# Performance work log

Measured on AMD Instinct MI355X. Metric: run time of the kernel, lower is better.

## Reference

```python
import jax, jax.numpy as jnp
import numpy as np

QMIN, QMAX = -128.0, 127.0  # int8 fake-quant range for activations
BIAS_ZP = 128.0             # zero point for the uint8-stored quantized bias


def ste_fake_quant(x, scale, zp):
    # scaled fake-quantize: q = clip(round(x/s) + zp, qmin, qmax); deq = (q - zp) * s
    q = jnp.clip(jnp.round(x / scale) + zp, QMIN, QMAX)
    deq = (q - zp) * scale
    # straight-through estimator (matches torch fake_quantize semantics)
    return x + jax.lax.stop_gradient(deq - x)


def setup_inputs() -> dict:
    key = jax.random.key(0)
    ks = jax.random.split(key, 8)
    B, S, K, N, G = 8, 8192, 1024, 1024, 128
    NG = K // G  # groups per output channel
    x = jax.random.normal(ks[0], (B, S, K), dtype=jnp.float32)
    w_q = jax.random.randint(ks[1], (N, K), 0, 16, dtype=jnp.int32)          # int4 codes
    w_scale = jax.random.uniform(ks[2], (N, NG), dtype=jnp.float32) * 0.02 + 1e-3
    w_zp = jax.random.randint(ks[3], (N, NG), 0, 16, dtype=jnp.int32)
    bias_q = jax.random.randint(ks[4], (N,), 0, 256, dtype=jnp.int32)        # uint8 codes
    bias_scale = jax.random.uniform(ks[5], (N,), dtype=jnp.float32) * 0.01 + 1e-4
    in_scale = jax.random.uniform(ks[6], (1,), dtype=jnp.float32) * 0.02 + 0.01
    in_zp = jnp.zeros((1,), dtype=jnp.int32)
    out_scale = jax.random.uniform(ks[7], (1,), dtype=jnp.float32) * 0.2 + 0.05
    out_zp = jnp.zeros((1,), dtype=jnp.int32)
    return {"x": x, "w_q": w_q, "w_scale": w_scale, "w_zp": w_zp,
            "bias_q": bias_q, "bias_scale": bias_scale,
            "in_scale": in_scale, "in_zp": in_zp,
            "out_scale": out_scale, "out_zp": out_zp}


def reference(x, w_q, w_scale, w_zp, bias_q, bias_scale, in_scale, in_zp, out_scale, out_zp):
    dt = x.dtype
    N, K = w_q.shape
    NG = w_scale.shape[1]
    G = K // NG
    # group-wise weight dequantize: [N, K] -> [N, NG, G]
    wq = w_q.reshape(N, NG, G).astype(dt)
    W = ((wq - w_zp[:, :, None].astype(dt)) * w_scale[:, :, None].astype(dt)).reshape(N, K)
    # per-channel bias dequantize
    bias = (bias_q.astype(dt) - BIAS_ZP) * bias_scale.astype(dt)
    # per-tensor fake-quantize of the input activation
    xq = ste_fake_quant(x, in_scale.astype(dt), in_zp.astype(dt))
    # func_method: linear
    out = jnp.einsum('bsk,nk->bsn', xq, W) + bias
    # per-tensor fake-quantize of the output
    return ste_fake_quant(out, out_scale.astype(dt), out_zp.astype(dt))
```

## Files before the change

kernel.cpp:

```cpp
#include <hip/hip_runtime.h>
#include <hip/hip_bf16.h>
#include <stdint.h>

#define M_DIM 65536
#define K_DIM 1024
#define N_DIM 1024
#define NGRP  8

#define T_BM 128
#define T_BN 128
#define T_BK 64
#define T_NKT (K_DIM / T_BK)

#define FB_BM 128
#define FB_BN 128
#define FB_BK 32
#define FB_NKT (K_DIM / FB_BK)

typedef float f32x4 __attribute__((ext_vector_type(4)));
typedef int   ix4   __attribute__((ext_vector_type(4)));
typedef __bf16 bf16x8 __attribute__((ext_vector_type(8)));

__global__ void prep_wd_kernel(const int* __restrict__ w_q,
                               const int* __restrict__ w_zp,
                               const int* __restrict__ bias_q,
                               const float* __restrict__ bias_scale,
                               int8_t* __restrict__ Wd,
                               float* __restrict__ bias_f) {
    const int n = blockIdx.x;
    const int t = threadIdx.x;
    const int k0 = t * 4;
    const int g = k0 >> 7;
    const int zp = w_zp[n * NGRP + g];
    const int4 wq = *reinterpret_cast<const int4*>(w_q + (size_t)n * K_DIM + k0);
    union { int u; int8_t b[4]; } pk;
    pk.b[0] = (int8_t)(wq.x - zp);
    pk.b[1] = (int8_t)(wq.y - zp);
    pk.b[2] = (int8_t)(wq.z - zp);
    pk.b[3] = (int8_t)(wq.w - zp);
    *reinterpret_cast<int*>(Wd + (size_t)n * K_DIM + k0) = pk.u;
    if (t == 0) bias_f[n] = ((float)bias_q[n] - 128.0f) * bias_scale[n];
}

__global__ __launch_bounds__(256) void prep_x8_kernel(
    const float* __restrict__ x,
    const float* __restrict__ in_scale_p, const int* __restrict__ in_zp_p,
    int8_t* __restrict__ Xq)
{
    const float s = in_scale_p[0];
    const float inv = 1.0f / s;
    const float zp = (float)in_zp_p[0];
    const size_t i = ((size_t)blockIdx.x * 256 + threadIdx.x) * 16;
    float vv[16];
#pragma unroll
    for (int c = 0; c < 4; ++c) {
        const float4 v = *reinterpret_cast<const float4*>(x + i + c * 4);
        vv[c * 4 + 0] = v.x; vv[c * 4 + 1] = v.y;
        vv[c * 4 + 2] = v.z; vv[c * 4 + 3] = v.w;
    }
    union { int4 u; int8_t b[16]; } pk;
#pragma unroll
    for (int e = 0; e < 16; ++e) {
        float q = rintf(vv[e] * inv) + zp;
        q = fminf(fmaxf(q, -128.0f), 127.0f);
        pk.b[e] = (int8_t)(q - zp);
    }
    *reinterpret_cast<int4*>(Xq + i) = pk.u;
}

__global__ __launch_bounds__(256, 3) void gemm128_i8_kernel(
    const int8_t* __restrict__ Xq,
    const int8_t* __restrict__ Wd,
    const float* __restrict__ w_scale,
    const float* __restrict__ bias_f,
    const float* __restrict__ in_scale_p,
    const float* __restrict__ out_scale_p, const int* __restrict__ out_zp_p,
    float* __restrict__ out)
{
    __shared__ __align__(16) int8_t Abuf[2][T_BM * T_BK];
    __shared__ __align__(16) int8_t Bbuf[2][T_BN * T_BK];
    __shared__ float WS[NGRP * T_BN];

    const int t = threadIdx.x;
    const int bid = (blockIdx.x & 7) * 512 + (blockIdx.x >> 3);
    const int nt = bid & 7;
    const int mt = bid >> 3;
    const int m0 = mt * T_BM;
    const int n0 = nt * T_BN;

    const int wid = t >> 6;
    const int lane = t & 63;
    const int wr = wid >> 1, wc = wid & 1;
    const int lrow = lane & 15;
    const int kslot = lane >> 4;
    const int koff = ((kslot ^ ((lrow >> 1) & 3)) << 4);
    const int widoff = wid * 1024;

    const int8_t* Abase = Xq + (size_t)m0 * K_DIM;
    const int8_t* Bbase = Wd + (size_t)n0 * K_DIM;

    {
        const int nl = t >> 1;
        const int g4 = (t & 1) * 4;
        const float4 wv = *reinterpret_cast<const float4*>(
            w_scale + (size_t)(n0 + nl) * NGRP + g4);
        WS[(g4 + 0) * T_BN + nl] = wv.x;
        WS[(g4 + 1) * T_BN + nl] = wv.y;
        WS[(g4 + 2) * T_BN + nl] = wv.z;
        WS[(g4 + 3) * T_BN + nl] = wv.w;
    }

    auto stage = [&](int8_t* dst, const int8_t* panel, int kt) {
        const int k0 = kt * T_BK;
#pragma unroll
        for (int j = 0; j < 2; ++j) {
            const int c = j * 256 + t;
            const int r = c >> 2;
            const int sl = (c & 3) ^ ((r >> 1) & 3);
            const int8_t* src = panel + (size_t)r * K_DIM + k0 + sl * 16;
            __builtin_amdgcn_global_load_lds(
                (const __attribute__((address_space(1))) void*)src,
                (__attribute__((address_space(3))) void*)(dst + j * 4096 + widoff),
                16, 0, 0);
        }
    };

    f32x4 facc[4][4];
#pragma unroll
    for (int mi = 0; mi < 4; ++mi)
#pragma unroll
        for (int ni = 0; ni < 4; ++ni)
            facc[mi][ni] = (f32x4){0.f, 0.f, 0.f, 0.f};

    stage(&Abuf[0][0], Abase, 0);
    stage(&Bbuf[0][0], Bbase, 0);
    __syncthreads();

    int buf = 0;
#pragma unroll 1
    for (int kt = 0; kt < T_NKT; ++kt) {
        if (kt + 1 < T_NKT) {
            stage(&Abuf[buf ^ 1][0], Abase, kt + 1);
            stage(&Bbuf[buf ^ 1][0], Bbase, kt + 1);
        }

        ix4 af[4], bfr[4];
#pragma unroll
        for (int i = 0; i < 4; ++i) {
            const int arow = wr * 64 + i * 16 + lrow;
            af[i] = *reinterpret_cast<const ix4*>(&Abuf[buf][arow * 64 + koff]);
        }
#pragma unroll
        for (int i = 0; i < 4; ++i) {
            const int brow = wc * 64 + i * 16 + lrow;
            bfr[i] = *reinterpret_cast<const ix4*>(&Bbuf[buf][brow * 64 + koff]);
        }

        const int g = kt >> 1;
        float wsv[4];
#pragma unroll
        for (int ni = 0; ni < 4; ++ni)
            wsv[ni] = WS[g * T_BN + wc * 64 + ni * 16 + lrow];

#pragma unroll
        for (int mi = 0; mi < 4; ++mi) {
            ix4 s0 = __builtin_amdgcn_mfma_i32_16x16x64_i8(af[mi], bfr[0], (ix4){0,0,0,0}, 0, 0, 0);
            ix4 s1 = __builtin_amdgcn_mfma_i32_16x16x64_i8(af[mi], bfr[1], (ix4){0,0,0,0}, 0, 0, 0);
            ix4 s2 = __builtin_amdgcn_mfma_i32_16x16x64_i8(af[mi], bfr[2], (ix4){0,0,0,0}, 0, 0, 0);
            ix4 s3 = __builtin_amdgcn_mfma_i32_16x16x64_i8(af[mi], bfr[3], (ix4){0,0,0,0}, 0, 0, 0);
#pragma unroll
            for (int e = 0; e < 4; ++e) {
                facc[mi][0][e] += wsv[0] * (float)s0[e];
                facc[mi][1][e] += wsv[1] * (float)s1[e];
                facc[mi][2][e] += wsv[2] * (float)s2[e];
                facc[mi][3][e] += wsv[3] * (float)s3[e];
            }
        }

        __syncthreads();
        buf ^= 1;
    }

    const float in_s  = in_scale_p[0];
    const float out_s = out_scale_p[0];
    const float out_inv = 1.0f / out_s;
    const float ozp = (float)out_zp_p[0];
    const int col = lane & 15;
    const int rgrp = lane >> 4;
#pragma unroll
    for (int ni = 0; ni < 4; ++ni) {
        const int n = n0 + wc * 64 + ni * 16 + col;
        const float bv = bias_f[n];
#pragma unroll
        for (int mi = 0; mi < 4; ++mi) {
#pragma unroll
            for (int j = 0; j < 4; ++j) {
                const int m = m0 + wr * 64 + mi * 16 + rgrp * 4 + j;
                float v = in_s * facc[mi][ni][j] + bv;
                float q = rintf(v * out_inv) + ozp;
                q = fminf(fmaxf(q, -128.0f), 127.0f);
                out[(size_t)m * N_DIM + n] = (q - ozp) * out_s;
            }
        }
    }
}

__global__ void prep_kernel(const int* __restrict__ w_q,
                            const float* __restrict__ w_scale,
                            const int* __restrict__ w_zp,
                            const int* __restrict__ bias_q,
                            const float* __restrict__ bias_scale,
                            __hip_bfloat16* __restrict__ Wb,
                            float* __restrict__ bias_f) {
    const int n = blockIdx.x;
    const int t = threadIdx.x;
    const int k0 = t * 4;
    const int g = k0 >> 7;
    const float s  = w_scale[n * NGRP + g];
    const float zp = (float)w_zp[n * NGRP + g];
    const int4 wq = *reinterpret_cast<const int4*>(w_q + (size_t)n * K_DIM + k0);
    union { ushort4 u; __hip_bfloat16 h[4]; } pk;
    pk.h[0] = __float2bfloat16(((float)wq.x - zp) * s);
    pk.h[1] = __float2bfloat16(((float)wq.y - zp) * s);
    pk.h[2] = __float2bfloat16(((float)wq.z - zp) * s);
    pk.h[3] = __float2bfloat16(((float)wq.w - zp) * s);
    *reinterpret_cast<ushort4*>(Wb + (size_t)n * K_DIM + k0) = pk.u;
    if (t == 0) bias_f[n] = ((float)bias_q[n] - 128.0f) * bias_scale[n];
}

__global__ __launch_bounds__(256) void gemm_fused_kernel(
    const float* __restrict__ x,
    const __hip_bfloat16* __restrict__ Wb,
    const float* __restrict__ bias_f,
    const float* __restrict__ in_scale_p, const int* __restrict__ in_zp_p,
    const float* __restrict__ out_scale_p, const int* __restrict__ out_zp_p,
    float* __restrict__ out)
{
    __shared__ __align__(16) __hip_bfloat16 As[2][FB_BM][FB_BK];
    __shared__ __align__(16) __hip_bfloat16 Bs[2][FB_BN][FB_BK];

    const int t = threadIdx.x;
    const int bid = blockIdx.x;
    const int nt = bid & 7;
    const int mt = bid >> 3;
    const int m0 = mt * FB_BM;
    const int n0 = nt * FB_BN;

    const int wid = t >> 6;
    const int lane = t & 63;
    const int wr = wid >> 1, wc = wid & 1;
    const int lrow = lane & 15;
    const int kslot = lane >> 4;

    const float in_s = in_scale_p[0];
    const float in_inv = 1.0f / in_s;
    const float izp = (float)in_zp_p[0];

    auto stageB = [&](int b, int kt) {
        const int k0 = kt * FB_BK;
#pragma unroll
        for (int j = 0; j < 2; ++j) {
            const int c = (wid * 2 + j) * 64 + lane;
            const int row = c >> 2;
            const int slot = c & 3;
            const __hip_bfloat16* src = Wb + (size_t)(n0 + row) * K_DIM + k0 + slot * 8;
            __builtin_amdgcn_global_load_lds(
                (const __attribute__((address_space(1))) void*)src,
                (__attribute__((address_space(3))) void*)((char*)&Bs[b][0][0] + (wid * 2 + j) * 1024),
                16, 0, 0);
        }
    };
    auto stageA = [&](int b, int kt) {
        const int k0 = kt * FB_BK;
#pragma unroll
        for (int i = 0; i < 4; ++i) {
            const int c = t + 256 * i;
            const int row = c >> 3;
            const int slot = c & 7;
            const float4 v = *reinterpret_cast<const float4*>(
                x + (size_t)(m0 + row) * K_DIM + k0 + slot * 4);
            float vv[4] = {v.x, v.y, v.z, v.w};
            union { ushort4 u; __hip_bfloat16 h[4]; } pk;
#pragma unroll
            for (int e = 0; e < 4; ++e) {
                float q = rintf(vv[e] * in_inv) + izp;
                q = fminf(fmaxf(q, -128.0f), 127.0f);
                pk.h[e] = __float2bfloat16((q - izp) * in_s);
            }
            *reinterpret_cast<ushort4*>(&As[b][row][slot * 4]) = pk.u;
        }
    };

    f32x4 acc[4][4];
#pragma unroll
    for (int mi = 0; mi < 4; ++mi)
#pragma unroll
        for (int ni = 0; ni < 4; ++ni)
            acc[mi][ni] = (f32x4){0.f, 0.f, 0.f, 0.f};

    stageB(0, 0);
    stageA(0, 0);
    __syncthreads();

    for (int kt = 0; kt < FB_NKT; ++kt) {
        const int buf = kt & 1;
        if (kt + 1 < FB_NKT) {
            stageB(buf ^ 1, kt + 1);
            stageA(buf ^ 1, kt + 1);
        }
        bf16x8 af[4], bfr[4];
#pragma unroll
        for (int mi = 0; mi < 4; ++mi)
            af[mi] = *reinterpret_cast<const bf16x8*>(&As[buf][wr * 64 + mi * 16 + lrow][kslot * 8]);
#pragma unroll
        for (int ni = 0; ni < 4; ++ni)
            bfr[ni] = *reinterpret_cast<const bf16x8*>(&Bs[buf][wc * 64 + ni * 16 + lrow][kslot * 8]);
#pragma unroll
        for (int mi = 0; mi < 4; ++mi)
#pragma unroll
            for (int ni = 0; ni < 4; ++ni)
                acc[mi][ni] = __builtin_amdgcn_mfma_f32_16x16x32_bf16(af[mi], bfr[ni], acc[mi][ni], 0, 0, 0);
        __syncthreads();
    }

    const float out_s = out_scale_p[0];
    const float out_inv = 1.0f / out_s;
    const float ozp = (float)out_zp_p[0];
    const int col = lane & 15;
    const int rgrp = lane >> 4;
#pragma unroll
    for (int ni = 0; ni < 4; ++ni) {
        const int n = n0 + wc * 64 + ni * 16 + col;
        const float bv = bias_f[n];
#pragma unroll
        for (int mi = 0; mi < 4; ++mi) {
#pragma unroll
            for (int j = 0; j < 4; ++j) {
                const int m = m0 + wr * 64 + mi * 16 + rgrp * 4 + j;
                float v = acc[mi][ni][j] + bv;
                float q = rintf(v * out_inv) + ozp;
                q = fminf(fmaxf(q, -128.0f), 127.0f);
                out[(size_t)m * N_DIM + n] = (q - ozp) * out_s;
            }
        }
    }
}

extern "C" void kernel_launch(void* const* d_in, const int* in_sizes, int n_in,
                              void* d_out, int out_size, void* d_ws, size_t ws_size,
                              hipStream_t stream) {
    const float* x          = (const float*)d_in[0];
    const int*   w_q        = (const int*)d_in[1];
    const float* w_scale    = (const float*)d_in[2];
    const int*   w_zp       = (const int*)d_in[3];
    const int*   bias_q     = (const int*)d_in[4];
    const float* bias_scale = (const float*)d_in[5];
    const float* in_scale   = (const float*)d_in[6];
    const int*   in_zp      = (const int*)d_in[7];
    const float* out_scale  = (const float*)d_in[8];
    const int*   out_zp     = (const int*)d_in[9];

    const size_t xq8_bytes = (size_t)M_DIM * K_DIM;
    const size_t wd_bytes  = (size_t)N_DIM * K_DIM;
    const size_t need = xq8_bytes + wd_bytes + N_DIM * sizeof(float);

    if (ws_size >= need) {
        int8_t* Xq8 = (int8_t*)d_ws;
        int8_t* Wd  = (int8_t*)((char*)d_ws + xq8_bytes);
        float* bias_f = (float*)((char*)d_ws + xq8_bytes + wd_bytes);

        prep_wd_kernel<<<N_DIM, 256, 0, stream>>>(w_q, w_zp, bias_q, bias_scale, Wd, bias_f);
        prep_x8_kernel<<<(int)(((size_t)M_DIM * K_DIM) / (256 * 16)), 256, 0, stream>>>(
            x, in_scale, in_zp, Xq8);

        const int grid = (M_DIM / T_BM) * (N_DIM / T_BN);
        gemm128_i8_kernel<<<grid, 256, 0, stream>>>(Xq8, Wd, w_scale, bias_f,
                                                    in_scale, out_scale, out_zp,
                                                    (float*)d_out);
    } else {
        __hip_bfloat16* Wb = (__hip_bfloat16*)d_ws;
        float* bias_f = (float*)((char*)d_ws + (size_t)N_DIM * K_DIM * sizeof(__hip_bfloat16));

        prep_kernel<<<N_DIM, 256, 0, stream>>>(w_q, w_scale, w_zp, bias_q, bias_scale, Wb, bias_f);
        const int grid = (M_DIM / FB_BM) * (N_DIM / FB_BN);
        gemm_fused_kernel<<<grid, 256, 0, stream>>>(x, Wb, bias_f, in_scale, in_zp,
                                                    out_scale, out_zp, (float*)d_out);
    }
}
```

Measured before the change: 223.4 us.

## Accumulate int32 MFMA across each quant group before float scaling

The K loop now walks one weight-quant group (two K tiles) per iteration. The int8 MFMA chains its int32 accumulator across both tiles, and the float scale-and-add runs once per group instead of once per tile. The input scale is folded into the shared weight-scale table, so the epilogue multiply goes away. The loop is manually unrolled with fixed buffer indices, and the occupancy hint of 3 blocks per CU is dropped. This may raise register pressure, since 16 ix4 int accumulators stay live alongside the float accumulators.

```diff
diff --git a/kernel.cpp b/kernel.cpp
--- a/kernel.cpp
+++ b/kernel.cpp
@@ -68,7 +68,7 @@
     *reinterpret_cast<int4*>(Xq + i) = pk.u;
 }
 
-__global__ __launch_bounds__(256, 3) void gemm128_i8_kernel(
+__global__ __launch_bounds__(256) void gemm128_i8g_kernel(
     const int8_t* __restrict__ Xq,
     const int8_t* __restrict__ Wd,
     const float* __restrict__ w_scale,
@@ -100,14 +100,15 @@
     const int8_t* Bbase = Wd + (size_t)n0 * K_DIM;
 
     {
+        const float in_s = in_scale_p[0];
         const int nl = t >> 1;
         const int g4 = (t & 1) * 4;
         const float4 wv = *reinterpret_cast<const float4*>(
             w_scale + (size_t)(n0 + nl) * NGRP + g4);
-        WS[(g4 + 0) * T_BN + nl] = wv.x;
-        WS[(g4 + 1) * T_BN + nl] = wv.y;
-        WS[(g4 + 2) * T_BN + nl] = wv.z;
-        WS[(g4 + 3) * T_BN + nl] = wv.w;
+        WS[(g4 + 0) * T_BN + nl] = wv.x * in_s;
+        WS[(g4 + 1) * T_BN + nl] = wv.y * in_s;
+        WS[(g4 + 2) * T_BN + nl] = wv.z * in_s;
+        WS[(g4 + 3) * T_BN + nl] = wv.w * in_s;
     }
 
     auto stage = [&](int8_t* dst, const int8_t* panel, int kt) {
@@ -136,52 +137,70 @@
     stage(&Bbuf[0][0], Bbase, 0);
     __syncthreads();
 
-    int buf = 0;
+    ix4 it0[4][4];
+
 #pragma unroll 1
-    for (int kt = 0; kt < T_NKT; ++kt) {
-        if (kt + 1 < T_NKT) {
-            stage(&Abuf[buf ^ 1][0], Abase, kt + 1);
-            stage(&Bbuf[buf ^ 1][0], Bbase, kt + 1);
-        }
-
-        ix4 af[4], bfr[4];
-#pragma unroll
-        for (int i = 0; i < 4; ++i) {
-            const int arow = wr * 64 + i * 16 + lrow;
-            af[i] = *reinterpret_cast<const ix4*>(&Abuf[buf][arow * 64 + koff]);
-        }
-#pragma unroll
-        for (int i = 0; i < 4; ++i) {
-            const int brow = wc * 64 + i * 16 + lrow;
-            bfr[i] = *reinterpret_cast<const ix4*>(&Bbuf[buf][brow * 64 + koff]);
-        }
-
-        const int g = kt >> 1;
-        float wsv[4];
-#pragma unroll
-        for (int ni = 0; ni < 4; ++ni)
-            wsv[ni] = WS[g * T_BN + wc * 64 + ni * 16 + lrow];
-
-#pragma unroll
-        for (int mi = 0; mi < 4; ++mi) {
-            ix4 s0 = __builtin_amdgcn_mfma_i32_16x16x64_i8(af[mi], bfr[0], (ix4){0,0,0,0}, 0, 0, 0);
-            ix4 s1 = __builtin_amdgcn_mfma_i32_16x16x64_i8(af[mi], bfr[1], (ix4){0,0,0,0}, 0, 0, 0);
-            ix4 s2 = __builtin_amdgcn_mfma_i32_16x16x64_i8(af[mi], bfr[2], (ix4){0,0,0,0}, 0, 0, 0);
-            ix4 s3 = __builtin_amdgcn_mfma_i32_16x16x64_i8(af[mi], bfr[3], (ix4){0,0,0,0}, 0, 0, 0);
-#pragma unroll
-            for (int e = 0; e < 4; ++e) {
-                facc[mi][0][e] += wsv[0] * (float)s0[e];
-                facc[mi][1][e] += wsv[1] * (float)s1[e];
-                facc[mi][2][e] += wsv[2] * (float)s2[e];
-                facc[mi][3][e] += wsv[3] * (float)s3[e];
-            }
-        }
-
+    for (int g = 0; g < NGRP; ++g) {
+        stage(&Abuf[1][0], Abase, 2 * g + 1);
+        stage(&Bbuf[1][0], Bbase, 2 * g + 1);
+        {
+            ix4 af[4], bfr[4];
+#pragma unroll
+            for (int i = 0; i < 4; ++i) {
+                const int arow = wr * 64 + i * 16 + lrow;
+                af[i] = *reinterpret_cast<const ix4*>(&Abuf[0][arow * 64 + koff]);
+            }
+#pragma unroll
+            for (int i = 0; i < 4; ++i) {
+                const int brow = wc * 64 + i * 16 + lrow;
+                bfr[i] = *reinterpret_cast<const ix4*>(&Bbuf[0][brow * 64 + koff]);
+            }
+#pragma unroll
+            for (int mi = 0; mi < 4; ++mi)
+#pragma unroll
+                for (int ni = 0; ni < 4; ++ni)
+                    it0[mi][ni] = __builtin_amdgcn_mfma_i32_16x16x64_i8(
+                        af[mi], bfr[ni], (ix4){0, 0, 0, 0}, 0, 0, 0);
+        }
         __syncthreads();
-        buf ^= 1;
-    }
-
-    const float in_s  = in_scale_p[0];
+
+        if (g + 1 < NGRP) {
+            stage(&Abuf[0][0], Abase, 2 * g + 2);
+            stage(&Bbuf[0][0], Bbase, 2 * g + 2);
+        }
+        {
+            ix4 af[4], bfr[4];
+#pragma unroll
+            for (int i = 0; i < 4; ++i) {
+                const int arow = wr * 64 + i * 16 + lrow;
+                af[i] = *reinterpret_cast<const ix4*>(&Abuf[1][arow * 64 + koff]);
+            }
+#pragma unroll
+            for (int i = 0; i < 4; ++i) {
+                const int brow = wc * 64 + i * 16 + lrow;
+                bfr[i] = *reinterpret_cast<const ix4*>(&Bbuf[1][brow * 64 + koff]);
+            }
+            float wsv[4];
+#pragma unroll
+            for (int ni = 0; ni < 4; ++ni)
+                wsv[ni] = WS[g * T_BN + wc * 64 + ni * 16 + lrow];
+#pragma unroll
+            for (int mi = 0; mi < 4; ++mi)
+#pragma unroll
+                for (int ni = 0; ni < 4; ++ni)
+                    it0[mi][ni] = __builtin_amdgcn_mfma_i32_16x16x64_i8(
+                        af[mi], bfr[ni], it0[mi][ni], 0, 0, 0);
+#pragma unroll
+            for (int mi = 0; mi < 4; ++mi)
+#pragma unroll
+                for (int ni = 0; ni < 4; ++ni)
+#pragma unroll
+                    for (int e = 0; e < 4; ++e)
+                        facc[mi][ni][e] += wsv[ni] * (float)it0[mi][ni][e];
+        }
+        __syncthreads();
+    }
+
     const float out_s = out_scale_p[0];
     const float out_inv = 1.0f / out_s;
     const float ozp = (float)out_zp_p[0];
@@ -196,7 +215,7 @@
 #pragma unroll
             for (int j = 0; j < 4; ++j) {
                 const int m = m0 + wr * 64 + mi * 16 + rgrp * 4 + j;
-                float v = in_s * facc[mi][ni][j] + bv;
+                float v = facc[mi][ni][j] + bv;
                 float q = rintf(v * out_inv) + ozp;
                 q = fminf(fmaxf(q, -128.0f), 127.0f);
                 out[(size_t)m * N_DIM + n] = (q - ozp) * out_s;
@@ -374,9 +393,9 @@
             x, in_scale, in_zp, Xq8);
 
         const int grid = (M_DIM / T_BM) * (N_DIM / T_BN);
-        gemm128_i8_kernel<<<grid, 256, 0, stream>>>(Xq8, Wd, w_scale, bias_f,
-                                                    in_scale, out_scale, out_zp,
-                                                    (float*)d_out);
+        gemm128_i8g_kernel<<<grid, 256, 0, stream>>>(Xq8, Wd, w_scale, bias_f,
+                                                     in_scale, out_scale, out_zp,
+                                                     (float*)d_out);
     } else {
         __hip_bfloat16* Wb = (__hip_bfloat16*)d_ws;
         float* bias_f = (float*)((char*)d_ws + (size_t)N_DIM * K_DIM * sizeof(__hip_bfloat16));
```

After: 266.2 us. 1.19x slower.
